# Performance work log

Measured on AMD Instinct MI355X. Metric: run time of the kernel, lower is better.

The kernel has to match this reference:

```python
import jax, jax.numpy as jnp
import numpy as np

HIDDEN = 4096
N_HEADS = 32
N_KV_HEADS = 8
HEAD_DIM = HIDDEN // N_HEADS  # 128
N_KV_GROUPS = N_HEADS // N_KV_HEADS  # 4
SEQ = 2048
BSZ = 1
ROPE_THETA = 10000.0


def _rope_cos_sin(seqlen, head_dim, dtype):
    # freqs_cis = polar(1, outer(t, theta^{-2i/d})) -> cos/sin tables [S, hd/2]
    inv_freq = 1.0 / (ROPE_THETA ** (jnp.arange(0, head_dim, 2, dtype=jnp.float32) / head_dim))
    t = jnp.arange(seqlen, dtype=jnp.float32)
    freqs = jnp.outer(t, inv_freq)  # [S, hd/2]
    return jnp.cos(freqs).astype(dtype), jnp.sin(freqs).astype(dtype)


def _apply_rotary(x, cos, sin):
    # x: [B, S, H, hd]. Torch code pairs (x[:hd/2], x[hd/2:]) as (real, imag):
    # out = concat(x1*cos - x2*sin, x1*sin + x2*cos)
    half = x.shape[-1] // 2
    x1, x2 = x[..., :half], x[..., half:]
    c = cos[None, :, None, :]  # [1, S, 1, hd/2]
    s = sin[None, :, None, :]
    return jnp.concatenate([x1 * c - x2 * s, x1 * s + x2 * c], axis=-1)


def setup_inputs() -> dict:
    key = jax.random.key(0)
    k1, k2, k3 = jax.random.split(key, 3)
    hidden_states = jax.random.normal(k1, (BSZ, SEQ, HIDDEN), dtype=jnp.float32)
    w_qkv = jax.random.normal(k2, (HIDDEN, (N_HEADS + 2 * N_KV_HEADS) * HEAD_DIM), dtype=jnp.float32) * 0.02
    w_o = jax.random.normal(k3, (HIDDEN, HIDDEN), dtype=jnp.float32) * 0.02
    # HF-style additive causal mask [1, 1, S, S]
    causal = jnp.tril(jnp.ones((SEQ, SEQ), dtype=bool))
    attention_mask = jnp.where(causal, 0.0, -1e9).astype(jnp.float32)[None, None]
    return {"hidden_states": hidden_states, "w_qkv": w_qkv, "w_o": w_o,
            "attention_mask": attention_mask}


def reference(hidden_states, w_qkv, w_o, attention_mask):
    bsz, seqlen, _ = hidden_states.shape
    # fused (dequantized) QKV projection
    xqkv = jnp.einsum('bsh,hd->bsd', hidden_states, w_qkv)
    xqkv = xqkv.reshape(bsz, seqlen, N_HEADS + 2 * N_KV_HEADS, HEAD_DIM)
    xq = xqkv[:, :, :N_HEADS]                      # [B, S, 32, 128]
    xk = xqkv[:, :, N_HEADS:N_HEADS + N_KV_HEADS]  # [B, S, 8, 128]
    xv = xqkv[:, :, -N_KV_HEADS:]                  # [B, S, 8, 128]

    cos, sin = _rope_cos_sin(seqlen, HEAD_DIM, hidden_states.dtype)
    xq = _apply_rotary(xq, cos, sin)
    xk = _apply_rotary(xk, cos, sin)

    # GQA: repeat_interleave kv heads along head dim
    keys = jnp.repeat(xk, N_KV_GROUPS, axis=2)    # [B, S, 32, 128]
    values = jnp.repeat(xv, N_KV_GROUPS, axis=2)

    q = xq.transpose(0, 2, 1, 3)   # [B, H, S, D]
    k = keys.transpose(0, 2, 1, 3)
    v = values.transpose(0, 2, 1, 3)

    scores = jnp.einsum('bhqd,bhkd->bhqk', q, k) / np.sqrt(HEAD_DIM)
    scores = scores + attention_mask
    probs = jax.nn.softmax(scores.astype(jnp.float32), axis=-1).astype(q.dtype)
    out = jnp.einsum('bhqk,bhkd->bhqd', probs, v)
    attention_weight = out.transpose(0, 2, 1, 3).reshape(bsz, seqlen, -1)
    attn_output = jnp.einsum('bsh,ho->bso', attention_weight, w_o)
    return attn_output
```

## Files before the change

### kernel.cpp

```cpp
#include <hip/hip_runtime.h>
#include <stdint.h>

typedef unsigned short u16;
typedef __bf16 bf8 __attribute__((ext_vector_type(8)));
typedef float f32x4 __attribute__((ext_vector_type(4)));

#define SEQ 2048
#define HIDDEN 4096
#define DQKV 6144
#define HD 128

#define GLOAD_LDS16(g, l)                                                            \
    __builtin_amdgcn_global_load_lds((const __attribute__((address_space(1))) void*)(g), \
                                     (__attribute__((address_space(3))) void*)(l), 16, 0, 0)

__device__ __forceinline__ u16 f2bf(float f) {
    union { float f; unsigned u; } v{f};
    unsigned r = (v.u + 0x7fff + ((v.u >> 16) & 1)) >> 16;
    return (u16)r;
}
__device__ __forceinline__ float bf2f(u16 b) {
    union { unsigned u; float f; } v;
    v.u = ((unsigned)b) << 16;
    return v.f;
}


__global__ void convert_bf16_kernel(const float* __restrict__ in, u16* __restrict__ out) {
    int i = (blockIdx.x * 256 + threadIdx.x) * 4;
    float4 v = *(const float4*)(in + i);
    u16 o[4] = {f2bf(v.x), f2bf(v.y), f2bf(v.z), f2bf(v.w)};
    *(uint2*)(out + i) = *(uint2*)o;
}

__global__ void transpose_w_kernel(const float* __restrict__ in, u16* __restrict__ out, int K, int N) {
    __shared__ u16 tile[64][65];
    int tn = N >> 6;
    int bk = blockIdx.x / tn, bn = blockIdx.x % tn;
    int k0 = bk * 64, n0 = bn * 64;
    int c = threadIdx.x & 63, r0 = threadIdx.x >> 6;
#pragma unroll
    for (int r = r0; r < 64; r += 4)
        tile[r][c] = f2bf(in[(size_t)(k0 + r) * N + n0 + c]);
    __syncthreads();
#pragma unroll
    for (int r = r0; r < 64; r += 4)
        out[(size_t)(n0 + r) * K + k0 + c] = tile[c][r];
}

__global__ void rope_kernel(u16* __restrict__ x) {
    const int row = blockIdx.x / 10, hg = blockIdx.x % 10;
    const int head = hg * 4 + (threadIdx.x >> 6), j = threadIdx.x & 63;
    u16* p = x + (size_t)row * DQKV + head * HD + j;
    float x1 = bf2f(p[0]), x2 = bf2f(p[64]);
    float inv = exp2f(-(float)j * 0.20762050593045952f);
    float s, c;
    sincosf((float)row * inv, &s, &c);
    p[0] = f2bf(x1 * c - x2 * s);
    p[64] = f2bf(x1 * s + x2 * c);
}

__global__ void transpose_v_kernel(const u16* __restrict__ xqkv, u16* __restrict__ vt) {
    __shared__ u16 tile[64][65];
    int h = blockIdx.x >> 6;
    int t = blockIdx.x & 63;
    int s0 = (t >> 1) * 64, d0 = (t & 1) * 64;
    int c = threadIdx.x & 63, r0 = threadIdx.x >> 6;
    const u16* src = xqkv + (40 + h) * HD + d0;
#pragma unroll
    for (int r = r0; r < 64; r += 4)
        tile[r][c] = src[(size_t)(s0 + r) * DQKV + c];
    __syncthreads();
    u16* dst = vt + ((size_t)h * HD + d0) * SEQ + s0;
#pragma unroll
    for (int r = r0; r < 64; r += 4)
        dst[(size_t)r * SEQ + c] = tile[c][r];
}

template <int MODE>
__global__ __launch_bounds__(256) void gemm_bt_kernel(const u16* __restrict__ A,
                                                      const u16* __restrict__ BT,
                                                      u16* __restrict__ Cbf,
                                                      float* __restrict__ Cf) {
    constexpr int NT = (MODE == 0) ? 6 : 8;
    constexpr int NROWS = NT * 16;
    constexpr int CSTR = (MODE == 0) ? DQKV : HIDDEN;
    __shared__ u16 lA[128][32];
    __shared__ u16 lB[NROWS][32];
    const int tid = threadIdx.x;
    const int w = tid >> 6, l = tid & 63, l15 = l & 15, q4 = l >> 4;
    const int bm = blockIdx.x & 15, bn = blockIdx.x >> 4;

    const u16* ga = A + (size_t)(bm * 128 + w * 32 + (l >> 2)) * 4096 + (l & 3) * 8;
    const u16* gb = BT + (size_t)(bn * NROWS + (l >> 2)) * 4096 + (l & 3) * 8;

    f32x4 acc[2][NT] = {};

    for (int kt = 0; kt < 128; ++kt) {
        __syncthreads();
        GLOAD_LDS16(ga, &lA[w * 32][0]);
        GLOAD_LDS16(ga + 16 * 4096, &lA[w * 32 + 16][0]);
#pragma unroll
        for (int c = w; c < NT; c += 4)
            GLOAD_LDS16(gb + (size_t)c * 16 * 4096, &lB[c * 16][0]);
        ga += 32; gb += 32;
        __syncthreads();
        bf8 af[2], bfr[NT];
#pragma unroll
        for (int mt = 0; mt < 2; ++mt)
            af[mt] = *(const bf8*)&lA[w * 32 + mt * 16 + l15][q4 * 8];
#pragma unroll
        for (int nt = 0; nt < NT; ++nt)
            bfr[nt] = *(const bf8*)&lB[nt * 16 + l15][q4 * 8];
#pragma unroll
        for (int mt = 0; mt < 2; ++mt)
#pragma unroll
            for (int nt = 0; nt < NT; ++nt)
                acc[mt][nt] = __builtin_amdgcn_mfma_f32_16x16x32_bf16(af[mt], bfr[nt], acc[mt][nt], 0, 0, 0);
    }

    const int rowbase = bm * 128 + w * 32;
    const int colbase = bn * NROWS;
#pragma unroll
    for (int mt = 0; mt < 2; ++mt)
#pragma unroll
        for (int nt = 0; nt < NT; ++nt)
#pragma unroll
            for (int r = 0; r < 4; ++r) {
                int row = rowbase + mt * 16 + q4 * 4 + r;
                int col = colbase + nt * 16 + l15;
                if constexpr (MODE == 0)
                    Cbf[(size_t)row * CSTR + col] = f2bf(acc[mt][nt][r]);
                else
                    Cf[(size_t)row * CSTR + col] = acc[mt][nt][r];
            }
}

#define PSTR 72
__global__ __launch_bounds__(256) void attn_kernel(const u16* __restrict__ xqkv,
                                                   const u16* __restrict__ vt,
                                                   u16* __restrict__ aw) {
    __shared__ __align__(16) u16 sm[16384 + 128 * PSTR];
    const int tid = threadIdx.x, w = tid >> 6, l = tid & 63, l15 = l & 15, q4 = l >> 4;
    const int qh = blockIdx.x & 31;
    const int qslot = blockIdx.x >> 5;
    const int qt = (qslot < 8) ? qslot : 23 - qslot;
    const int kh = qh >> 2;

    {
        const u16* gq = xqkv + (size_t)(qt * 128 + (l >> 2)) * DQKV + qh * HD + w * 32 + (l & 3) * 8;
#pragma unroll
        for (int i = 0; i < 8; ++i)
            GLOAD_LDS16(gq + (size_t)i * 16 * DQKV, &sm[w * 4096 + i * 512]);
    }
    __syncthreads();
    bf8 qf[4][2];
#pragma unroll
    for (int ks = 0; ks < 4; ++ks)
#pragma unroll
        for (int mt = 0; mt < 2; ++mt)
            qf[ks][mt] = *(const bf8*)&sm[ks * 4096 + (w * 32 + mt * 16 + l15) * 32 + q4 * 8];
    __syncthreads();

    f32x4 O[2][8] = {};
    float plrow[2][4] = {};

    u16* ldsK = sm;
    u16* ldsV = sm + 8192;
    u16* ldsP = sm + 16384;
    const int nkt = 2 * qt + 2;
    const float cs = 0.12751744f;

    const u16* gk_base = xqkv + (32 + kh) * HD + w * 32 + (l & 3) * 8;
    const u16* gv_base = vt + (size_t)kh * HD * SEQ + (size_t)((w & 1) * 64 + (l >> 2)) * SEQ + (w >> 1) * 32 + (l & 3) * 8;

    for (int kt = 0; kt < nkt; ++kt) {
        {
            const u16* gk = gk_base + (size_t)(kt * 64 + (l >> 2)) * DQKV;
#pragma unroll
            for (int i = 0; i < 4; ++i)
                GLOAD_LDS16(gk + (size_t)i * 16 * DQKV, ldsK + w * 2048 + i * 512);
        }
        {
            const u16* gv = gv_base + kt * 64;
#pragma unroll
            for (int i = 0; i < 4; ++i)
                GLOAD_LDS16(gv + (size_t)i * 16 * SEQ, ldsV + (w >> 1) * 4096 + (w & 1) * 2048 + i * 512);
        }
        __syncthreads();

        f32x4 S[2][4] = {};
#pragma unroll
        for (int ks = 0; ks < 4; ++ks) {
            bf8 kf[4];
#pragma unroll
            for (int nt = 0; nt < 4; ++nt)
                kf[nt] = *(const bf8*)&ldsK[ks * 2048 + (nt * 16 + l15) * 32 + q4 * 8];
#pragma unroll
            for (int mt = 0; mt < 2; ++mt)
#pragma unroll
                for (int nt = 0; nt < 4; ++nt)
                    S[mt][nt] = __builtin_amdgcn_mfma_f32_16x16x32_bf16(qf[ks][mt], kf[nt], S[mt][nt], 0, 0, 0);
        }

        const bool domask = (kt >= 2 * qt);
#pragma unroll
        for (int mt = 0; mt < 2; ++mt)
#pragma unroll
            for (int r = 0; r < 4; ++r) {
                const int row = qt * 128 + w * 32 + mt * 16 + q4 * 4 + r;
#pragma unroll
                for (int nt = 0; nt < 4; ++nt) {
                    float t = S[mt][nt][r] * cs;
                    if (domask && (kt * 64 + nt * 16 + l15 > row)) t = -1e30f;
                    float p = exp2f(t);
                    plrow[mt][r] += p;
                    ldsP[(w * 32 + mt * 16 + q4 * 4 + r) * PSTR + nt * 16 + l15] = f2bf(p);
                }
            }

#pragma unroll
        for (int pk = 0; pk < 2; ++pk) {
            bf8 pf[2], vf[8];
#pragma unroll
            for (int mt = 0; mt < 2; ++mt)
                pf[mt] = *(const bf8*)&ldsP[(w * 32 + mt * 16 + l15) * PSTR + pk * 32 + q4 * 8];
#pragma unroll
            for (int nt = 0; nt < 8; ++nt)
                vf[nt] = *(const bf8*)&ldsV[pk * 4096 + (nt * 16 + l15) * 32 + q4 * 8];
#pragma unroll
            for (int mt = 0; mt < 2; ++mt)
#pragma unroll
                for (int nt = 0; nt < 8; ++nt)
                    O[mt][nt] = __builtin_amdgcn_mfma_f32_16x16x32_bf16(pf[mt], vf[nt], O[mt][nt], 0, 0, 0);
        }
        __syncthreads();
    }

#pragma unroll
    for (int mt = 0; mt < 2; ++mt)
#pragma unroll
        for (int r = 0; r < 4; ++r) {
            float ls = plrow[mt][r];
#pragma unroll
            for (int off = 1; off <= 8; off <<= 1)
                ls += __shfl_xor(ls, off, 64);
            const float linv = 1.0f / ls;
            const int row = qt * 128 + w * 32 + mt * 16 + q4 * 4 + r;
#pragma unroll
            for (int nt = 0; nt < 8; ++nt)
                aw[(size_t)row * 4096 + qh * HD + nt * 16 + l15] = f2bf(O[mt][nt][r] * linv);
        }
}


extern "C" void kernel_launch(void* const* d_in, const int* in_sizes, int n_in,
                              void* d_out, int out_size, void* d_ws, size_t ws_size,
                              hipStream_t stream) {
    const float* hs = (const float*)d_in[0];
    const float* wqkv = (const float*)d_in[1];
    const float* wo = (const float*)d_in[2];
    float* out = (float*)d_out;

    char* ws = (char*)d_ws;
    const size_t oHbf = 0;
    const size_t oWqkvT = oHbf + (size_t)SEQ * HIDDEN * 2;
    const size_t oWoT = oWqkvT + (size_t)DQKV * HIDDEN * 2;
    const size_t oXQKV = oWoT + (size_t)HIDDEN * HIDDEN * 2;
    const size_t oVT = oXQKV + (size_t)SEQ * DQKV * 2;
    const size_t oAW = oVT + (size_t)8 * HD * SEQ * 2;
    const size_t total = oAW + (size_t)SEQ * HIDDEN * 2;
    if (ws_size < total) return;

    u16* Hbf = (u16*)(ws + oHbf);
    u16* WqkvT = (u16*)(ws + oWqkvT);
    u16* WoT = (u16*)(ws + oWoT);
    u16* XQKV = (u16*)(ws + oXQKV);
    u16* VT = (u16*)(ws + oVT);
    u16* AW = (u16*)(ws + oAW);

    convert_bf16_kernel<<<(SEQ * HIDDEN) / 1024, 256, 0, stream>>>(hs, Hbf);
    transpose_w_kernel<<<(HIDDEN / 64) * (DQKV / 64), 256, 0, stream>>>(wqkv, WqkvT, HIDDEN, DQKV);
    transpose_w_kernel<<<(HIDDEN / 64) * (HIDDEN / 64), 256, 0, stream>>>(wo, WoT, HIDDEN, HIDDEN);
    gemm_bt_kernel<0><<<16 * 64, 256, 0, stream>>>(Hbf, WqkvT, XQKV, nullptr);
    rope_kernel<<<SEQ * 10, 256, 0, stream>>>(XQKV);
    transpose_v_kernel<<<8 * 64, 256, 0, stream>>>(XQKV, VT);
    attn_kernel<<<512, 256, 0, stream>>>(XQKV, VT, AW);
    gemm_bt_kernel<1><<<16 * 32, 256, 0, stream>>>(AW, WoT, nullptr, out);
}
```

Before: 574.1 us.

## Replace GEMM with 256x256-tile 8-wave double-buffered pipelined kernel

Replaces the 128xN single-buffered GEMM with a 512-thread kernel that computes 256x256 output tiles. It uses a K-step of 64, double-buffered LDS staged via global_load_lds, XOR-swizzled LDS layout, and a ping-pong barrier/setprio schedule that interleaves LDS reads with MFMA bursts. The aim is more data reuse per loaded byte and hiding global-load latency behind compute. In exchange it uses far fewer workgroups (192 and 128), which may underfill the 256 CUs and cause tail imbalance, and it adds heavy register use for the 32 accumulators per wave.

```diff
diff --git a/kernel.cpp b/kernel.cpp
--- a/kernel.cpp
+++ b/kernel.cpp
@@ -78,61 +78,167 @@
 }
 
 template <int MODE>
-__global__ __launch_bounds__(256) void gemm_bt_kernel(const u16* __restrict__ A,
-                                                      const u16* __restrict__ BT,
-                                                      u16* __restrict__ Cbf,
-                                                      float* __restrict__ Cf) {
-    constexpr int NT = (MODE == 0) ? 6 : 8;
-    constexpr int NROWS = NT * 16;
+__global__ __launch_bounds__(512, 2) void gemm8p_kernel(const u16* __restrict__ A,
+                                                        const u16* __restrict__ BT,
+                                                        u16* __restrict__ Cbf,
+                                                        float* __restrict__ Cf) {
+    constexpr int NBT = (MODE == 0) ? 24 : 16;
     constexpr int CSTR = (MODE == 0) ? DQKV : HIDDEN;
-    __shared__ u16 lA[128][32];
-    __shared__ u16 lB[NROWS][32];
+    constexpr int NT = 4096 / 64;
+    __shared__ u16 lds[2][4][8192];
     const int tid = threadIdx.x;
     const int w = tid >> 6, l = tid & 63, l15 = l & 15, q4 = l >> 4;
-    const int bm = blockIdx.x & 15, bn = blockIdx.x >> 4;
-
-    const u16* ga = A + (size_t)(bm * 128 + w * 32 + (l >> 2)) * 4096 + (l & 3) * 8;
-    const u16* gb = BT + (size_t)(bn * NROWS + (l >> 2)) * 4096 + (l & 3) * 8;
-
-    f32x4 acc[2][NT] = {};
-
-    for (int kt = 0; kt < 128; ++kt) {
-        __syncthreads();
-        GLOAD_LDS16(ga, &lA[w * 32][0]);
-        GLOAD_LDS16(ga + 16 * 4096, &lA[w * 32 + 16][0]);
-#pragma unroll
-        for (int c = w; c < NT; c += 4)
-            GLOAD_LDS16(gb + (size_t)c * 16 * 4096, &lB[c * 16][0]);
-        ga += 32; gb += 32;
-        __syncthreads();
-        bf8 af[2], bfr[NT];
-#pragma unroll
-        for (int mt = 0; mt < 2; ++mt)
-            af[mt] = *(const bf8*)&lA[w * 32 + mt * 16 + l15][q4 * 8];
-#pragma unroll
-        for (int nt = 0; nt < NT; ++nt)
-            bfr[nt] = *(const bf8*)&lB[nt * 16 + l15][q4 * 8];
-#pragma unroll
-        for (int mt = 0; mt < 2; ++mt)
-#pragma unroll
-            for (int nt = 0; nt < NT; ++nt)
-                acc[mt][nt] = __builtin_amdgcn_mfma_f32_16x16x32_bf16(af[mt], bfr[nt], acc[mt][nt], 0, 0, 0);
+    const int wm = w >> 2, wn = w & 3;
+    const int bm = blockIdx.x / NBT, bn = blockIdx.x % NBT;
+
+    const char* sp[8];
+    {
+        const int r0 = tid >> 3;
+        const int cb = ((tid & 7) << 4) ^ (((tid >> 5) & 1) << 5);
+#pragma unroll
+        for (int h = 0; h < 4; ++h)
+#pragma unroll
+            for (int i = 0; i < 2; ++i) {
+                const u16* base = (h < 2)
+                    ? A + (size_t)(bm * 256 + h * 128 + r0 + i * 64) * 4096
+                    : BT + (size_t)(bn * 256 + (h - 2) * 128 + r0 + i * 64) * 4096;
+                sp[h * 2 + i] = (const char*)base + cb;
+            }
     }
 
-    const int rowbase = bm * 128 + w * 32;
-    const int colbase = bn * NROWS;
-#pragma unroll
-    for (int mt = 0; mt < 2; ++mt)
-#pragma unroll
-        for (int nt = 0; nt < NT; ++nt)
+#define STAGE8(b)                                                                  \
+    do {                                                                           \
+        _Pragma("unroll") for (int h = 0; h < 4; ++h)                              \
+            _Pragma("unroll") for (int i = 0; i < 2; ++i)                          \
+                GLOAD_LDS16(sp[h * 2 + i], &lds[b][h][w * 512 + i * 4096]);        \
+        _Pragma("unroll") for (int j = 0; j < 8; ++j) sp[j] += 128;                \
+    } while (0)
+
+    f32x4 acc[8][4] = {};
+
+    STAGE8(0);
+    STAGE8(1);
+    asm volatile("s_waitcnt vmcnt(8)" ::: "memory");
+    asm volatile("s_barrier" ::: "memory");
+
+    const int smask = ((l15 >> 2) & 1) << 5;
+    const int c0 = (q4 * 16) ^ smask;
+    const int c1 = (64 + q4 * 16) ^ smask;
+    const int lrb = (wn & 1) * 64;
+
+#pragma unroll 1
+    for (int tt = 0; tt < NT; tt += 2) {
+#pragma unroll
+        for (int half = 0; half < 2; ++half) {
+            const int t = tt + half;
+            const int cur = half;
+            const char* ha = (const char*)&lds[cur][wm][0];
+            const char* hb = (const char*)&lds[cur][2 + (wn >> 1)][0];
+            bf8 a[4][2], b0[2][2], b1[2][2];
+
+#pragma unroll
+            for (int mf = 0; mf < 4; ++mf) {
+                const int lr = mf * 16 + l15;
+                a[mf][0] = *(const bf8*)(ha + lr * 128 + c0);
+                a[mf][1] = *(const bf8*)(ha + lr * 128 + c1);
+            }
+#pragma unroll
+            for (int nf = 0; nf < 2; ++nf) {
+                const int lr = lrb + nf * 16 + l15;
+                b0[nf][0] = *(const bf8*)(hb + lr * 128 + c0);
+                b0[nf][1] = *(const bf8*)(hb + lr * 128 + c1);
+            }
+            asm volatile("s_barrier" ::: "memory");
+            asm volatile("s_waitcnt lgkmcnt(0)" ::: "memory");
+            __builtin_amdgcn_s_setprio(1);
+#pragma unroll
+            for (int mf = 0; mf < 4; ++mf)
+#pragma unroll
+                for (int nf = 0; nf < 2; ++nf)
+#pragma unroll
+                    for (int ks = 0; ks < 2; ++ks)
+                        acc[mf][nf] = __builtin_amdgcn_mfma_f32_16x16x32_bf16(
+                            a[mf][ks], b0[nf][ks], acc[mf][nf], 0, 0, 0);
+            __builtin_amdgcn_s_setprio(0);
+            asm volatile("s_barrier" ::: "memory");
+
+#pragma unroll
+            for (int nf = 0; nf < 2; ++nf) {
+                const int lr = lrb + (2 + nf) * 16 + l15;
+                b1[nf][0] = *(const bf8*)(hb + lr * 128 + c0);
+                b1[nf][1] = *(const bf8*)(hb + lr * 128 + c1);
+            }
+            asm volatile("s_barrier" ::: "memory");
+            asm volatile("s_waitcnt lgkmcnt(0)" ::: "memory");
+            __builtin_amdgcn_s_setprio(1);
+#pragma unroll
+            for (int mf = 0; mf < 4; ++mf)
+#pragma unroll
+                for (int nf = 0; nf < 2; ++nf)
+#pragma unroll
+                    for (int ks = 0; ks < 2; ++ks)
+                        acc[mf][2 + nf] = __builtin_amdgcn_mfma_f32_16x16x32_bf16(
+                            a[mf][ks], b1[nf][ks], acc[mf][2 + nf], 0, 0, 0);
+            __builtin_amdgcn_s_setprio(0);
+            asm volatile("s_barrier" ::: "memory");
+
+#pragma unroll
+            for (int mf = 0; mf < 4; ++mf) {
+                const int lr = (4 + mf) * 16 + l15;
+                a[mf][0] = *(const bf8*)(ha + lr * 128 + c0);
+                a[mf][1] = *(const bf8*)(ha + lr * 128 + c1);
+            }
+            asm volatile("s_barrier" ::: "memory");
+            asm volatile("s_waitcnt lgkmcnt(0)" ::: "memory");
+            __builtin_amdgcn_s_setprio(1);
+#pragma unroll
+            for (int mf = 0; mf < 4; ++mf)
+#pragma unroll
+                for (int nf = 0; nf < 2; ++nf)
+#pragma unroll
+                    for (int ks = 0; ks < 2; ++ks)
+                        acc[4 + mf][2 + nf] = __builtin_amdgcn_mfma_f32_16x16x32_bf16(
+                            a[mf][ks], b1[nf][ks], acc[4 + mf][2 + nf], 0, 0, 0);
+            __builtin_amdgcn_s_setprio(0);
+            asm volatile("s_barrier" ::: "memory");
+
+            __builtin_amdgcn_s_setprio(1);
+#pragma unroll
+            for (int mf = 0; mf < 4; ++mf)
+#pragma unroll
+                for (int nf = 0; nf < 2; ++nf)
+#pragma unroll
+                    for (int ks = 0; ks < 2; ++ks)
+                        acc[4 + mf][nf] = __builtin_amdgcn_mfma_f32_16x16x32_bf16(
+                            a[mf][ks], b0[nf][ks], acc[4 + mf][nf], 0, 0, 0);
+            __builtin_amdgcn_s_setprio(0);
+            asm volatile("s_barrier" ::: "memory");
+
+            if (t < NT - 2) {
+                STAGE8(cur);
+                asm volatile("s_waitcnt vmcnt(8)" ::: "memory");
+            } else if (t == NT - 2) {
+                asm volatile("s_waitcnt vmcnt(0)" ::: "memory");
+            }
+            asm volatile("s_barrier" ::: "memory");
+        }
+    }
+#undef STAGE8
+
+    const int rowb = bm * 256 + wm * 128;
+    const int colb = bn * 256 + wn * 64;
+#pragma unroll
+    for (int mf = 0; mf < 8; ++mf)
+#pragma unroll
+        for (int nf = 0; nf < 4; ++nf)
 #pragma unroll
             for (int r = 0; r < 4; ++r) {
-                int row = rowbase + mt * 16 + q4 * 4 + r;
-                int col = colbase + nt * 16 + l15;
+                const int row = rowb + mf * 16 + q4 * 4 + r;
+                const int col = colb + nf * 16 + l15;
                 if constexpr (MODE == 0)
-                    Cbf[(size_t)row * CSTR + col] = f2bf(acc[mt][nt][r]);
+                    Cbf[(size_t)row * CSTR + col] = f2bf(acc[mf][nf][r]);
                 else
-                    Cf[(size_t)row * CSTR + col] = acc[mt][nt][r];
+                    Cf[(size_t)row * CSTR + col] = acc[mf][nf][r];
             }
 }
 
@@ -282,9 +388,9 @@
     convert_bf16_kernel<<<(SEQ * HIDDEN) / 1024, 256, 0, stream>>>(hs, Hbf);
     transpose_w_kernel<<<(HIDDEN / 64) * (DQKV / 64), 256, 0, stream>>>(wqkv, WqkvT, HIDDEN, DQKV);
     transpose_w_kernel<<<(HIDDEN / 64) * (HIDDEN / 64), 256, 0, stream>>>(wo, WoT, HIDDEN, HIDDEN);
-    gemm_bt_kernel<0><<<16 * 64, 256, 0, stream>>>(Hbf, WqkvT, XQKV, nullptr);
+    gemm8p_kernel<0><<<8 * 24, 512, 0, stream>>>(Hbf, WqkvT, XQKV, nullptr);
     rope_kernel<<<SEQ * 10, 256, 0, stream>>>(XQKV);
     transpose_v_kernel<<<8 * 64, 256, 0, stream>>>(XQKV, VT);
     attn_kernel<<<512, 256, 0, stream>>>(XQKV, VT, AW);
-    gemm_bt_kernel<1><<<16 * 32, 256, 0, stream>>>(AW, WoT, nullptr, out);
-}
+    gemm8p_kernel<1><<<8 * 16, 512, 0, stream>>>(AW, WoT, nullptr, out);
+}
```

After: 635.3 us. 10.7% more time.

## Replace GEMM kernels with 8-wave double-buffered swizzled-LDS pipelined GEMM

Applied to the files above, without the earlier changes.

Both projection GEMMs move to a new 512-thread kernel with larger block tiles (256x192 for QKV, 128x256 for the output projection). It uses a BK=64 double-buffered LDS with an XOR swizzle and prefetches tiles two steps ahead. Global-to-LDS loads are interleaved into the MFMA phases, with explicit vmcnt waits, barriers and setprio. The aim is to hide global-load latency, avoid LDS bank conflicts and get more data reuse per tile than the old single-buffered kernel with two barriers per step. In exchange the grids are small (256 blocks) and the hand-tuned wait counts are fragile.

```diff
diff --git a/kernel.cpp b/kernel.cpp
--- a/kernel.cpp
+++ b/kernel.cpp
@@ -77,62 +77,130 @@
         dst[(size_t)r * SEQ + c] = tile[c][r];
 }
 
-template <int MODE>
-__global__ __launch_bounds__(256) void gemm_bt_kernel(const u16* __restrict__ A,
-                                                      const u16* __restrict__ BT,
-                                                      u16* __restrict__ Cbf,
-                                                      float* __restrict__ Cf) {
-    constexpr int NT = (MODE == 0) ? 6 : 8;
-    constexpr int NROWS = NT * 16;
+template <int BM, int BN, int MODE>
+__global__ __launch_bounds__(512, 2) void gemm8p_kernel(const u16* __restrict__ A,
+                                                        const u16* __restrict__ BT,
+                                                        u16* __restrict__ Cbf,
+                                                        float* __restrict__ Cf) {
+    constexpr int WM = BM / 32;
+    constexpr int WN = BN / 64;
+    constexpr int MP = WM / 4;
+    constexpr int NLA = BM / 64, NLB = BN / 64, NL = NLA + NLB;
+    constexpr int NBN = ((MODE == 0) ? DQKV : HIDDEN) / BN;
     constexpr int CSTR = (MODE == 0) ? DQKV : HIDDEN;
-    __shared__ u16 lA[128][32];
-    __shared__ u16 lB[NROWS][32];
+    constexpr int NT = 64;
+    __shared__ __align__(16) u16 lds[2][(BM + BN) * 64];
+
     const int tid = threadIdx.x;
     const int w = tid >> 6, l = tid & 63, l15 = l & 15, q4 = l >> 4;
-    const int bm = blockIdx.x & 15, bn = blockIdx.x >> 4;
-
-    const u16* ga = A + (size_t)(bm * 128 + w * 32 + (l >> 2)) * 4096 + (l & 3) * 8;
-    const u16* gb = BT + (size_t)(bn * NROWS + (l >> 2)) * 4096 + (l & 3) * 8;
-
-    f32x4 acc[2][NT] = {};
-
-    for (int kt = 0; kt < 128; ++kt) {
-        __syncthreads();
-        GLOAD_LDS16(ga, &lA[w * 32][0]);
-        GLOAD_LDS16(ga + 16 * 4096, &lA[w * 32 + 16][0]);
-#pragma unroll
-        for (int c = w; c < NT; c += 4)
-            GLOAD_LDS16(gb + (size_t)c * 16 * 4096, &lB[c * 16][0]);
-        ga += 32; gb += 32;
-        __syncthreads();
-        bf8 af[2], bfr[NT];
-#pragma unroll
-        for (int mt = 0; mt < 2; ++mt)
-            af[mt] = *(const bf8*)&lA[w * 32 + mt * 16 + l15][q4 * 8];
-#pragma unroll
-        for (int nt = 0; nt < NT; ++nt)
-            bfr[nt] = *(const bf8*)&lB[nt * 16 + l15][q4 * 8];
-#pragma unroll
-        for (int mt = 0; mt < 2; ++mt)
-#pragma unroll
-            for (int nt = 0; nt < NT; ++nt)
-                acc[mt][nt] = __builtin_amdgcn_mfma_f32_16x16x32_bf16(af[mt], bfr[nt], acc[mt][nt], 0, 0, 0);
+    const int wm = w >> 2, wn = w & 3;
+    const int bm = blockIdx.x / NBN, bn = blockIdx.x % NBN;
+
+    const int srow = tid >> 3;
+    const int scol = ((tid & 7) ^ ((tid >> 3) & 7)) << 4;
+    const char* spA[NLA];
+    const char* spB[NLB];
+#pragma unroll
+    for (int L = 0; L < NLA; ++L)
+        spA[L] = (const char*)(A + (size_t)(bm * BM + L * 64 + srow) * 4096) + scol;
+#pragma unroll
+    for (int L = 0; L < NLB; ++L)
+        spB[L] = (const char*)(BT + (size_t)(bn * BN + L * 64 + srow) * 4096) + scol;
+
+#define STG_A(L, tt, b) GLOAD_LDS16(spA[L] + (size_t)(tt) * 128, &lds[b][(L) * 4096 + w * 512])
+#define STG_B(L, tt, b) GLOAD_LDS16(spB[L] + (size_t)(tt) * 128, &lds[b][BM * 64 + (L) * 4096 + w * 512])
+
+#pragma unroll
+    for (int L = 0; L < NLA; ++L) STG_A(L, 0, 0);
+#pragma unroll
+    for (int L = 0; L < NLB; ++L) STG_B(L, 0, 0);
+#pragma unroll
+    for (int L = 0; L < NLA; ++L) STG_A(L, 1, 1);
+#pragma unroll
+    for (int L = 0; L < NLB; ++L) STG_B(L, 1, 1);
+    if constexpr (NL == 7) asm volatile("s_waitcnt vmcnt(7)" ::: "memory");
+    else                   asm volatile("s_waitcnt vmcnt(6)" ::: "memory");
+    asm volatile("s_barrier" ::: "memory");
+
+    const int c0x = (q4 * 16) ^ ((l15 & 7) << 4);
+    const int c1x = (64 + q4 * 16) ^ ((l15 & 7) << 4);
+
+    f32x4 acc[WM][WN] = {};
+    bf8 breg[WN][2];
+
+#pragma unroll 1
+    for (int t = 0; t < NT; ++t) {
+        const int cur = t & 1;
+        const char* ldsA = (const char*)&lds[cur][0];
+        const char* ldsB = ldsA + BM * 128;
+#pragma unroll
+        for (int p = 0; p < 4; ++p) {
+            if (p == 1 && t < NT - 2) {
+#pragma unroll
+                for (int L = 0; L < NLB; ++L) STG_B(L, t + 2, cur);
+            }
+            if constexpr (BM == 256) {
+                if (p == 2 && t < NT - 2) {
+                    STG_A(0, t + 2, cur);
+                    STG_A(2, t + 2, cur);
+                }
+            }
+            bf8 areg[MP][2];
+#pragma unroll
+            for (int j = 0; j < MP; ++j) {
+                const char* rp = ldsA + (wm * (BM / 2) + (p * MP + j) * 16 + l15) * 128;
+                areg[j][0] = *(const bf8*)(rp + c0x);
+                areg[j][1] = *(const bf8*)(rp + c1x);
+            }
+            if (p == 0) {
+#pragma unroll
+                for (int nf = 0; nf < WN; ++nf) {
+                    const char* rp = ldsB + (wn * (WN * 16) + nf * 16 + l15) * 128;
+                    breg[nf][0] = *(const bf8*)(rp + c0x);
+                    breg[nf][1] = *(const bf8*)(rp + c1x);
+                }
+            }
+            asm volatile("s_barrier" ::: "memory");
+            asm volatile("s_waitcnt lgkmcnt(0)" ::: "memory");
+            __builtin_amdgcn_s_setprio(1);
+#pragma unroll
+            for (int j = 0; j < MP; ++j)
+#pragma unroll
+                for (int nf = 0; nf < WN; ++nf)
+#pragma unroll
+                    for (int ks = 0; ks < 2; ++ks)
+                        acc[p * MP + j][nf] = __builtin_amdgcn_mfma_f32_16x16x32_bf16(
+                            areg[j][ks], breg[nf][ks], acc[p * MP + j][nf], 0, 0, 0);
+            __builtin_amdgcn_s_setprio(0);
+            asm volatile("s_barrier" ::: "memory");
+        }
+        if (t < NT - 2) {
+            if constexpr (BM == 256) { STG_A(1, t + 2, cur); STG_A(3, t + 2, cur); }
+            else                     { STG_A(0, t + 2, cur); STG_A(1, t + 2, cur); }
+            if constexpr (NL == 7) asm volatile("s_waitcnt vmcnt(7)" ::: "memory");
+            else                   asm volatile("s_waitcnt vmcnt(6)" ::: "memory");
+        } else if (t == NT - 2) {
+            asm volatile("s_waitcnt vmcnt(0)" ::: "memory");
+        }
+        asm volatile("s_barrier" ::: "memory");
     }
-
-    const int rowbase = bm * 128 + w * 32;
-    const int colbase = bn * NROWS;
-#pragma unroll
-    for (int mt = 0; mt < 2; ++mt)
-#pragma unroll
-        for (int nt = 0; nt < NT; ++nt)
+#undef STG_A
+#undef STG_B
+
+    const int rowb = bm * BM + wm * (BM / 2);
+    const int colb = bn * BN + wn * (WN * 16);
+#pragma unroll
+    for (int mf = 0; mf < WM; ++mf)
+#pragma unroll
+        for (int nf = 0; nf < WN; ++nf)
 #pragma unroll
             for (int r = 0; r < 4; ++r) {
-                int row = rowbase + mt * 16 + q4 * 4 + r;
-                int col = colbase + nt * 16 + l15;
+                const int row = rowb + mf * 16 + q4 * 4 + r;
+                const int col = colb + nf * 16 + l15;
                 if constexpr (MODE == 0)
-                    Cbf[(size_t)row * CSTR + col] = f2bf(acc[mt][nt][r]);
+                    Cbf[(size_t)row * CSTR + col] = f2bf(acc[mf][nf][r]);
                 else
-                    Cf[(size_t)row * CSTR + col] = acc[mt][nt][r];
+                    Cf[(size_t)row * CSTR + col] = acc[mf][nf][r];
             }
 }
 
@@ -282,9 +350,9 @@
     convert_bf16_kernel<<<(SEQ * HIDDEN) / 1024, 256, 0, stream>>>(hs, Hbf);
     transpose_w_kernel<<<(HIDDEN / 64) * (DQKV / 64), 256, 0, stream>>>(wqkv, WqkvT, HIDDEN, DQKV);
     transpose_w_kernel<<<(HIDDEN / 64) * (HIDDEN / 64), 256, 0, stream>>>(wo, WoT, HIDDEN, HIDDEN);
-    gemm_bt_kernel<0><<<16 * 64, 256, 0, stream>>>(Hbf, WqkvT, XQKV, nullptr);
+    gemm8p_kernel<256, 192, 0><<<8 * 32, 512, 0, stream>>>(Hbf, WqkvT, XQKV, nullptr);
     rope_kernel<<<SEQ * 10, 256, 0, stream>>>(XQKV);
     transpose_v_kernel<<<8 * 64, 256, 0, stream>>>(XQKV, VT);
     attn_kernel<<<512, 256, 0, stream>>>(XQKV, VT, AW);
-    gemm_bt_kernel<1><<<16 * 32, 256, 0, stream>>>(AW, WoT, nullptr, out);
-}
+    gemm8p_kernel<128, 256, 1><<<16 * 16, 512, 0, stream>>>(AW, WoT, nullptr, out);
+}
```

New measurement: 519.3 us. 1.11x faster.
